# Kernel optimization log

Measured on AMD Instinct MI355X. Metric: run time of the kernel, lower is better.

## Reference

```python
import jax, jax.numpy as jnp
import numpy as np

N, IN, HID, OUT, HEADS = 50000, 128, 128, 16, 4
EL, EG = 800000, 200000
NEG_SLOPE = 0.2


def setup_inputs() -> dict:
    key = jax.random.key(0)
    ks = jax.random.split(key, 24)
    def gn(k, shape, fan_in):
        return (jax.random.normal(k, shape, jnp.float32) / np.sqrt(fan_in)).astype(jnp.float32)
    inp = {}
    inp['x'] = jax.random.normal(ks[0], (N, IN), jnp.float32)
    inp['local_edge_index'] = jax.random.randint(ks[1], (2, EL), 0, N, jnp.int64 if jax.config.jax_enable_x64 else jnp.int32)
    inp['global_edge_index'] = jax.random.randint(ks[2], (2, EG), 0, N, jnp.int64 if jax.config.jax_enable_x64 else jnp.int32)
    # local_processor: Linear(IN, HID)
    inp['W1'] = gn(ks[3], (IN, HID), IN); inp['b1'] = jnp.zeros((HID,), jnp.float32)
    # GCNConv(HID, HID): weight + bias
    inp['Wg'] = gn(ks[4], (HID, HID), HID); inp['bg'] = jnp.zeros((HID,), jnp.float32)
    # GATConv(HID, HID, heads=4, concat=False): lin to HEADS*HID, att vectors, bias of size HID
    inp['Wa'] = gn(ks[5], (HID, HEADS * HID), HID)
    inp['att_src'] = gn(ks[6], (HEADS, HID), HID)
    inp['att_dst'] = gn(ks[7], (HEADS, HID), HID)
    inp['ba'] = jnp.zeros((HID,), jnp.float32)
    # hierarchical_pool: Linear(2*HID, HID)
    inp['Wp'] = gn(ks[8], (2 * HID, HID), 2 * HID); inp['bp'] = jnp.zeros((HID,), jnp.float32)
    # classifier: Linear(HID, HID//2) -> ReLU -> Linear(HID//2, OUT)
    inp['Wc1'] = gn(ks[9], (HID, HID // 2), HID); inp['bc1'] = jnp.zeros((HID // 2,), jnp.float32)
    inp['Wc2'] = gn(ks[10], (HID // 2, OUT), HID // 2); inp['bc2'] = jnp.zeros((OUT,), jnp.float32)
    # uncertainty_head: Linear(HID, OUT)
    inp['Wu'] = gn(ks[11], (HID, OUT), HID); inp['bu'] = jnp.zeros((OUT,), jnp.float32)
    return inp


def _add_self_loops(ei, n):
    loop = jnp.arange(n, dtype=ei.dtype)
    return jnp.concatenate([ei[0], loop]), jnp.concatenate([ei[1], loop])


def gcn_conv(x, ei, W, b):
    n = x.shape[0]
    xw = x @ W                                        # [N, HID]
    src, dst = _add_self_loops(ei, n)
    deg = jax.ops.segment_sum(jnp.ones_like(dst, dtype=xw.dtype), dst, num_segments=n)
    dinv = jax.lax.rsqrt(jnp.maximum(deg, 1e-12))     # deg >= 1 thanks to self-loops
    norm = dinv[src] * dinv[dst]                      # [E+N]
    msg = xw[src] * norm[:, None]                     # gather + scale
    return jax.ops.segment_sum(msg, dst, num_segments=n) + b


def gat_conv(x, ei, W, att_src, att_dst, b):
    n = x.shape[0]
    h, c = att_src.shape
    xw = (x @ W).reshape(n, h, c)                     # [N, H, C]
    a_s = jnp.einsum('nhc,hc->nh', xw, att_src)       # [N, H]
    a_d = jnp.einsum('nhc,hc->nh', xw, att_dst)
    src, dst = _add_self_loops(ei, n)
    e = jax.nn.leaky_relu(a_s[src] + a_d[dst], NEG_SLOPE)   # [E+N, H]
    emax = jax.ops.segment_max(e, dst, num_segments=n)      # stable edge-softmax per dst
    ee = jnp.exp(e - emax[dst])
    denom = jax.ops.segment_sum(ee, dst, num_segments=n)
    alpha = ee / (denom[dst] + 1e-16)                        # [E+N, H]
    out = jax.ops.segment_sum(xw[src] * alpha[:, :, None], dst, num_segments=n)  # [N,H,C]
    return out.mean(axis=1) + b                              # concat=False -> head mean


def reference(x, local_edge_index, global_edge_index, W1, b1, Wg, bg, Wa, att_src, att_dst, ba, Wp, bp, Wc1, bc1, Wc2, bc2, Wu, bu):
    x_local = jax.nn.relu(x @ W1 + b1)                       # dropout is identity in eval
    x_lg = jax.nn.relu(gcn_conv(x_local, local_edge_index, Wg, bg))
    x_gg = jax.nn.relu(gat_conv(x_local, global_edge_index, Wa, att_src, att_dst, ba))
    x_comb = jnp.concatenate([x_lg, x_gg], axis=1)           # [N, 2*HID]
    x_pooled = jax.nn.relu(x_comb @ Wp + bp)
    x_final = x_pooled.mean(axis=0, keepdims=True)           # batch=None path
    prediction = jax.nn.relu(x_final @ Wc1 + bc1) @ Wc2 + bc2
    uncertainty = jax.nn.sigmoid(x_final @ Wu + bu)
    return prediction, uncertainty
```

## Files before the change

### kernel.cpp

```cpp
#include <hip/hip_runtime.h>
#include <hip/hip_bf16.h>

#define N_NODES 50000
#define F_IN 128
#define HID 128
#define N_OUT 16
#define HEADS 4
#define EL 800000
#define EG 200000
#define NEG_SLOPE 0.2f
#define NB 196
#define GB 391

typedef short bf16x8 __attribute__((ext_vector_type(8)));
typedef float f32x4 __attribute__((ext_vector_type(4)));
typedef float f32x2 __attribute__((ext_vector_type(2)));

static __device__ __forceinline__ float lrelu(float x) {
    return x > 0.f ? x : NEG_SLOPE * x;
}
static __device__ __forceinline__ unsigned short f2b(float f) {
    __hip_bfloat16 h = __float2bfloat16(f);
    return *reinterpret_cast<unsigned short*>(&h);
}
static __device__ __forceinline__ unsigned char f2fp8(float f) {
    unsigned pk = __builtin_amdgcn_cvt_pk_fp8_f32(f, f, 0, false);
    return (unsigned char)(pk & 0xFF);
}
static __device__ __forceinline__ f32x2 fp8x2_to_f32(unsigned u) {
    return __builtin_amdgcn_cvt_pk_f32_fp8((int)u, false);
}
static __device__ __forceinline__ float rdlane_f(float v, int l) {
    return __int_as_float(__builtin_amdgcn_readlane(__float_as_int(v), l));
}

__global__ __launch_bounds__(256) void conv_hist(
    const float* __restrict__ W1, unsigned short* __restrict__ W1t,
    const float* __restrict__ Wg, unsigned short* __restrict__ Wgt,
    const float* __restrict__ Wa, unsigned short* __restrict__ Wat,
    const float* __restrict__ Wp, unsigned short* __restrict__ Wpt,
    const int* __restrict__ ldst, const int* __restrict__ gdst, int* __restrict__ ghist)
{
    int b = blockIdx.x, t = threadIdx.x;
    if (b < 64) {
        int idx = b * 256 + t;
        int k = idx >> 7, n = idx & 127;
        W1t[n * 128 + k] = f2b(W1[idx]);
    } else if (b < 128) {
        int idx = (b - 64) * 256 + t;
        int k = idx >> 7, n = idx & 127;
        Wgt[n * 128 + k] = f2b(Wg[idx]);
    } else if (b < 384) {
        int idx = (b - 128) * 256 + t;
        int k = idx >> 9, n = idx & 511;
        Wat[(size_t)n * 128 + k] = f2b(Wa[idx]);
    } else if (b < 512) {
        int idx = (b - 384) * 256 + t;
        int k = idx >> 7, n = idx & 127;
        Wpt[(size_t)n * 256 + k] = f2b(Wp[idx]);
    } else {
        __shared__ int lh[NB];
        int blk = b - 512;
        bool loc = blk < 196;
        const int* dstp = loc ? ldst : gdst;
        int nE = loc ? EL : EG;
        int* gh = ghist + (loc ? 0 : NB);
        int start = (loc ? blk : blk - 196) * 4096;
        if (t < NB) lh[t] = 0;
        __syncthreads();
        #pragma unroll
        for (int i = 0; i < 16; i++) {
            int e = start + i * 256 + t;
            if (e < nE) atomicAdd(&lh[dstp[e] >> 8], 1);
        }
        __syncthreads();
        if (t < NB && lh[t]) atomicAdd(&gh[t], lh[t]);
    }
}

__global__ __launch_bounds__(256) void scan_gemmx(
    const int* __restrict__ ghist, int* __restrict__ bbase, int* __restrict__ gcur,
    const float* __restrict__ A, const unsigned short* __restrict__ Bt,
    const float* __restrict__ bias, unsigned short* __restrict__ out, int M)
{
    __shared__ unsigned short As[128 * 128];
    __shared__ unsigned short Bs[128 * 128];
    int tid = threadIdx.x;
    if (blockIdx.x < 2) {
        int* s = (int*)As;
        int g = blockIdx.x, t = tid;
        int v = (t < NB) ? ghist[g * NB + t] : 0;
        s[t] = v;
        __syncthreads();
        for (int off = 1; off < 256; off <<= 1) {
            int u = (t >= off) ? s[t - off] : 0;
            __syncthreads();
            s[t] += u;
            __syncthreads();
        }
        if (t < NB) {
            bbase[g * (NB + 1) + t] = s[t] - v;
            gcur[g * NB + t] = s[t] - v;
        }
        if (t == NB - 1) bbase[g * (NB + 1) + NB] = s[t];
        return;
    }
    int lane = tid & 63, w = tid >> 6;
    int wr = w >> 1, wc = w & 1;
    int l16 = lane & 15, lhi = lane >> 4;
    int m0 = (blockIdx.x - 2) * 128;
    f32x4 acc[4][4] = {};
    #pragma unroll
    for (int i = 0; i < 8; i++) {
        int u = tid + i * 256;
        int row = u >> 4, e0 = (u & 15) << 3;
        int sw = e0 ^ ((row & 7) << 3);
        int gr = m0 + row;
        unsigned short pb[8] = {};
        if (gr < M) {
            float4 a0 = *(const float4*)(A + (size_t)gr * 128 + e0);
            float4 a1 = *(const float4*)(A + (size_t)gr * 128 + e0 + 4);
            pb[0] = f2b(a0.x); pb[1] = f2b(a0.y); pb[2] = f2b(a0.z); pb[3] = f2b(a0.w);
            pb[4] = f2b(a1.x); pb[5] = f2b(a1.y); pb[6] = f2b(a1.z); pb[7] = f2b(a1.w);
        }
        *(bf16x8*)(As + row * 128 + sw) = *(bf16x8*)pb;
        bf16x8 vb = *(const bf16x8*)(Bt + (size_t)row * 128 + e0);
        *(bf16x8*)(Bs + row * 128 + sw) = vb;
    }
    __syncthreads();
    #pragma unroll
    for (int kk = 0; kk < 4; kk++) {
        int ke = kk * 32 + lhi * 8;
        bf16x8 af[4], bfr[4];
        #pragma unroll
        for (int m = 0; m < 4; m++) {
            int r = wr * 64 + m * 16 + l16;
            af[m] = *(const bf16x8*)(As + r * 128 + (ke ^ ((r & 7) << 3)));
        }
        #pragma unroll
        for (int n = 0; n < 4; n++) {
            int r = wc * 64 + n * 16 + l16;
            bfr[n] = *(const bf16x8*)(Bs + r * 128 + (ke ^ ((r & 7) << 3)));
        }
        #pragma unroll
        for (int m = 0; m < 4; m++)
            #pragma unroll
            for (int n = 0; n < 4; n++)
                acc[m][n] = __builtin_amdgcn_mfma_f32_16x16x32_bf16(af[m], bfr[n], acc[m][n], 0, 0, 0);
    }
    #pragma unroll
    for (int m = 0; m < 4; m++) {
        #pragma unroll
        for (int r = 0; r < 4; r++) {
            int row_g = m0 + wr * 64 + m * 16 + lhi * 4 + r;
            if (row_g >= M) continue;
            #pragma unroll
            for (int n = 0; n < 4; n++) {
                int col_g = wc * 64 + n * 16 + l16;
                float v = fmaxf(acc[m][n][r] + bias[col_g], 0.f);
                out[(size_t)row_g * 128 + col_g] = f2b(v);
            }
        }
    }
}

__global__ __launch_bounds__(256) void bucket_part(
    const int* __restrict__ lsrc, const int* __restrict__ ldst,
    const int* __restrict__ gsrc, const int* __restrict__ gdst,
    int* __restrict__ gcur, unsigned* __restrict__ ebuf_l, unsigned* __restrict__ ebuf_g)
{
    __shared__ int lhist[NB], lbase[NB];
    int blk = blockIdx.x, t = threadIdx.x;
    bool loc = blk < 196;
    const int* srcp = loc ? lsrc : gsrc;
    const int* dstp = loc ? ldst : gdst;
    int nE = loc ? EL : EG;
    unsigned* ebuf = loc ? ebuf_l : ebuf_g;
    int* cur = gcur + (loc ? 0 : NB);
    int start = (loc ? blk : blk - 196) * 4096;
    if (t < NB) lhist[t] = 0;
    __syncthreads();
    unsigned pk[16];
    #pragma unroll
    for (int i = 0; i < 16; i++) {
        int e = start + i * 256 + t;
        if (e < nE) {
            unsigned d = (unsigned)dstp[e];
            pk[i] = (d << 16) | (unsigned)srcp[e];
            atomicAdd(&lhist[d >> 8], 1);
        } else pk[i] = 0xFFFFFFFFu;
    }
    __syncthreads();
    if (t < NB) lbase[t] = atomicAdd(&cur[t], lhist[t]);
    __syncthreads();
    if (t < NB) lhist[t] = 0;
    __syncthreads();
    #pragma unroll
    for (int i = 0; i < 16; i++) {
        unsigned b = pk[i] >> 24;
        if (b < NB) {
            int r = atomicAdd(&lhist[b], 1);
            ebuf[lbase[b] + r] = pk[i];
        }
    }
}
__global__ __launch_bounds__(256) void bucket_csr(
    const unsigned* __restrict__ ebuf_l, const unsigned* __restrict__ ebuf_g,
    const int* __restrict__ bbase,
    int* __restrict__ offs_l, int* __restrict__ offs_g,
    unsigned short* __restrict__ csr_l, unsigned short* __restrict__ csr_g,
    float* __restrict__ dinv)
{
    __shared__ int cnt[256], s[256], cur[256];
    int blk = blockIdx.x, t = threadIdx.x;
    bool loc = blk < 196;
    int b = loc ? blk : blk - 196;
    const unsigned* ebuf = loc ? ebuf_l : ebuf_g;
    const int* bb = bbase + (loc ? 0 : NB + 1);
    int* offs = loc ? offs_l : offs_g;
    unsigned short* csr = loc ? csr_l : csr_g;
    int rs = bb[b], re = bb[b + 1];
    cnt[t] = 0;
    __syncthreads();
    for (int i = rs + t; i < re; i += 256) atomicAdd(&cnt[(ebuf[i] >> 16) & 255], 1);
    __syncthreads();
    int v = cnt[t];
    s[t] = v;
    __syncthreads();
    for (int off = 1; off < 256; off <<= 1) {
        int u = (t >= off) ? s[t - off] : 0;
        __syncthreads();
        s[t] += u;
        __syncthreads();
    }
    int excl = s[t] - v;
    int node = b * 256 + t;
    cur[t] = rs + excl;
    if (node < N_NODES) {
        offs[node] = rs + excl;
        if (loc) dinv[node] = rsqrtf((float)(v + 1));
    }
    if (blk == 0 && t == 0) offs_l[N_NODES] = EL;
    if (blk == 196 && t == 0) offs_g[N_NODES] = EG;
    __syncthreads();
    for (int i = rs + t; i < re; i += 256) {
        unsigned pk = ebuf[i];
        int r = atomicAdd(&cur[(pk >> 16) & 255], 1);
        csr[r] = (unsigned short)(pk & 0xFFFFu);
    }
}

__global__ __launch_bounds__(256) void gemm_gw5(
    const unsigned short* __restrict__ A, const unsigned short* __restrict__ Wgt,
    const unsigned short* __restrict__ Wat,
    unsigned char* __restrict__ xw_g8, unsigned char* __restrict__ xw_a8, int M,
    const float* __restrict__ atts, const float* __restrict__ attd,
    float* __restrict__ a_s, float* __restrict__ a_d,
    const float* __restrict__ dinv)
{
    __shared__ unsigned short As[128 * 128];
    __shared__ unsigned short Bs[128 * 128];
    __shared__ float sas[128], sad[128];
    int tid = threadIdx.x;
    int lane = tid & 63, w = tid >> 6;
    int wr = w >> 1, wc = w & 1;
    int l16 = lane & 15, lhi = lane >> 4;
    int m0 = blockIdx.x * 128;
    #pragma unroll
    for (int i = 0; i < 8; i++) {
        int u = tid + i * 256;
        int row = u >> 4, e0 = (u & 15) << 3;
        int sw = e0 ^ ((row & 7) << 3);
        bf16x8 va = {};
        int gr = m0 + row;
        if (gr < M) va = *(const bf16x8*)(A + (size_t)gr * 128 + e0);
        *(bf16x8*)(As + row * 128 + sw) = va;
    }
    for (int p = 0; p < 5; p++) {
        const unsigned short* Bt = (p == 0) ? Wgt : (Wat + (size_t)(p - 1) * 128 * 128);
        __syncthreads();
        #pragma unroll
        for (int i = 0; i < 8; i++) {
            int u = tid + i * 256;
            int row = u >> 4, e0 = (u & 15) << 3;
            int sw = e0 ^ ((row & 7) << 3);
            bf16x8 vb = *(const bf16x8*)(Bt + (size_t)row * 128 + e0);
            *(bf16x8*)(Bs + row * 128 + sw) = vb;
        }
        if (tid < 128) { sas[tid] = 0.f; sad[tid] = 0.f; }
        __syncthreads();
        f32x4 acc[4][4] = {};
        #pragma unroll
        for (int kk = 0; kk < 4; kk++) {
            int ke = kk * 32 + lhi * 8;
            bf16x8 af[4], bfr[4];
            #pragma unroll
            for (int m = 0; m < 4; m++) {
                int r = wr * 64 + m * 16 + l16;
                af[m] = *(const bf16x8*)(As + r * 128 + (ke ^ ((r & 7) << 3)));
            }
            #pragma unroll
            for (int n = 0; n < 4; n++) {
                int r = wc * 64 + n * 16 + l16;
                bfr[n] = *(const bf16x8*)(Bs + r * 128 + (ke ^ ((r & 7) << 3)));
            }
            #pragma unroll
            for (int m = 0; m < 4; m++)
                #pragma unroll
                for (int n = 0; n < 4; n++)
                    acc[m][n] = __builtin_amdgcn_mfma_f32_16x16x32_bf16(af[m], bfr[n], acc[m][n], 0, 0, 0);
        }
        if (p == 0) {
            #pragma unroll
            for (int m = 0; m < 4; m++)
                #pragma unroll
                for (int r = 0; r < 4; r++) {
                    int row_g = m0 + wr * 64 + m * 16 + lhi * 4 + r;
                    if (row_g >= M) continue;
                    float dv = dinv[row_g];
                    #pragma unroll
                    for (int n = 0; n < 4; n++) {
                        int col_g = wc * 64 + n * 16 + l16;
                        xw_g8[(size_t)row_g * 128 + col_g] = f2fp8(acc[m][n][r] * dv);
                    }
                }
        } else {
            int head = p - 1;
            float ats[4], atd[4];
            #pragma unroll
            for (int n = 0; n < 4; n++) {
                int cl = wc * 64 + n * 16 + l16;
                ats[n] = atts[head * 128 + cl];
                atd[n] = attd[head * 128 + cl];
            }
            #pragma unroll
            for (int m = 0; m < 4; m++) {
                #pragma unroll
                for (int r = 0; r < 4; r++) {
                    int row_l = wr * 64 + m * 16 + lhi * 4 + r;
                    int row_g = m0 + row_l;
                    float ps = 0.f, pd = 0.f;
                    #pragma unroll
                    for (int n = 0; n < 4; n++) {
                        float v = acc[m][n][r];
                        ps = fmaf(v, ats[n], ps);
                        pd = fmaf(v, atd[n], pd);
                        if (row_g < M) {
                            int col_g = head * 128 + wc * 64 + n * 16 + l16;
                            xw_a8[(size_t)row_g * 512 + col_g] = f2fp8(v);
                        }
                    }
                    #pragma unroll
                    for (int off = 1; off < 16; off <<= 1) {
                        ps += __shfl_xor(ps, off);
                        pd += __shfl_xor(pd, off);
                    }
                    if (l16 == 0) {
                        atomicAdd(&sas[row_l], ps);
                        atomicAdd(&sad[row_l], pd);
                    }
                }
            }
            __syncthreads();
            if (tid < 128) {
                int row_g = m0 + tid;
                if (row_g < M) {
                    a_s[(size_t)row_g * 4 + head] = sas[tid];
                    a_d[(size_t)row_g * 4 + head] = sad[tid];
                }
            }
        }
    }
}

__global__ __launch_bounds__(256) void fused_gather(
    const int* __restrict__ offs_l, const unsigned short* __restrict__ csr_l,
    const unsigned char* __restrict__ xw_g8, const float* __restrict__ dinv,
    const float* __restrict__ bg,
    const int* __restrict__ offs_g, const unsigned short* __restrict__ csr_g,
    const float* __restrict__ a_s, const float* __restrict__ a_d,
    const unsigned char* __restrict__ xw_a8, const float* __restrict__ ba,
    unsigned short* __restrict__ xcomb)
{
    int blk = blockIdx.x;
    int tid = threadIdx.x;
    int lane = tid & 63;
    int g = lane >> 4, q = lane & 15;
    if (blk < 12500) {
        int d = (blk * 256 + tid) >> 6;
        if (d >= N_NODES) return;
        int base = offs_l[d], end = offs_l[d + 1];
        unsigned goff = (unsigned)q * 8u;
        f32x2 a0 = {0.f, 0.f}, a1 = {0.f, 0.f}, a2 = {0.f, 0.f}, a3 = {0.f, 0.f};
        for (int i = base; i < end; ) {
            int chunk = min(64, end - i);
            int sv = (lane < chunk) ? (int)csr_l[i + lane] : 0;
            int nst = (chunk + 3) >> 2;
            int j = 0;
            for (; j + 2 <= nst; j += 2) {
                int eA = j * 4 + g, eB = eA + 4;
                int sA = __shfl(sv, eA);
                int sB = __shfl(sv, eB);
                float mkA = (eA < chunk) ? 1.f : 0.f;
                float mkB = (eB < chunk) ? 1.f : 0.f;
                uint2 vA = *(const uint2*)(xw_g8 + (((unsigned)sA) << 7) + goff);
                uint2 vB = *(const uint2*)(xw_g8 + (((unsigned)sB) << 7) + goff);
                f32x2 mA = {mkA, mkA}, mB = {mkB, mkB};
                a0 += __builtin_amdgcn_cvt_pk_f32_fp8((int)vA.x, false) * mA;
                a1 += __builtin_amdgcn_cvt_pk_f32_fp8((int)vA.x, true) * mA;
                a2 += __builtin_amdgcn_cvt_pk_f32_fp8((int)vA.y, false) * mA;
                a3 += __builtin_amdgcn_cvt_pk_f32_fp8((int)vA.y, true) * mA;
                a0 += __builtin_amdgcn_cvt_pk_f32_fp8((int)vB.x, false) * mB;
                a1 += __builtin_amdgcn_cvt_pk_f32_fp8((int)vB.x, true) * mB;
                a2 += __builtin_amdgcn_cvt_pk_f32_fp8((int)vB.y, false) * mB;
                a3 += __builtin_amdgcn_cvt_pk_f32_fp8((int)vB.y, true) * mB;
            }
            for (; j < nst; j++) {
                int e = j * 4 + g;
                int s = __shfl(sv, e);
                float mk = (e < chunk) ? 1.f : 0.f;
                f32x2 m2 = {mk, mk};
                uint2 v = *(const uint2*)(xw_g8 + (((unsigned)s) << 7) + goff);
                a0 += __builtin_amdgcn_cvt_pk_f32_fp8((int)v.x, false) * m2;
                a1 += __builtin_amdgcn_cvt_pk_f32_fp8((int)v.x, true) * m2;
                a2 += __builtin_amdgcn_cvt_pk_f32_fp8((int)v.y, false) * m2;
                a3 += __builtin_amdgcn_cvt_pk_f32_fp8((int)v.y, true) * m2;
            }
            i += chunk;
        }
        float av[8] = {a0[0], a0[1], a1[0], a1[1], a2[0], a2[1], a3[0], a3[1]};
        #pragma unroll
        for (int k = 0; k < 8; k++) {
            av[k] += __shfl_xor(av[k], 16);
            av[k] += __shfl_xor(av[k], 32);
        }
        if (g == 0) {
            float dd = dinv[d];
            uint2 sv2 = *(const uint2*)(xw_g8 + (((unsigned)d) << 7) + goff);
            f32x2 s0 = fp8x2_to_f32(sv2.x & 0xFFFFu);
            f32x2 s1 = __builtin_amdgcn_cvt_pk_f32_fp8((int)sv2.x, true);
            f32x2 s2 = fp8x2_to_f32(sv2.y & 0xFFFFu);
            f32x2 s3 = __builtin_amdgcn_cvt_pk_f32_fp8((int)sv2.y, true);
            float sf[8] = {s0[0], s0[1], s1[0], s1[1], s2[0], s2[1], s3[0], s3[1]};
            float4 b0 = *(const float4*)(bg + q * 8);
            float4 b1 = *(const float4*)(bg + q * 8 + 4);
            float bb[8] = {b0.x, b0.y, b0.z, b0.w, b1.x, b1.y, b1.z, b1.w};
            unsigned o[4];
            #pragma unroll
            for (int k = 0; k < 4; k++) {
                float v0 = fmaxf(dd * (av[2 * k] + sf[2 * k]) + bb[2 * k], 0.f);
                float v1 = fmaxf(dd * (av[2 * k + 1] + sf[2 * k + 1]) + bb[2 * k + 1], 0.f);
                o[k] = (unsigned)f2b(v0) | ((unsigned)f2b(v1) << 16);
            }
            *(uint4*)(xcomb + (size_t)d * 256 + q * 8) = make_uint4(o[0], o[1], o[2], o[3]);
        }
    } else {
        int d = ((blk - 12500) * 256 + tid) >> 6;
        if (d >= N_NODES) return;
        int base = offs_g[d], end = offs_g[d + 1];
        int deg = end - base;
        if (deg <= 16) {
            float ad_g = a_d[(size_t)d * 4 + g];
            float es = lrelu(a_s[(size_t)d * 4 + g] + ad_g);
            int sv = (q < deg) ? (int)csr_g[base + q] : 0;
            float asg = a_s[(size_t)sv * 4 + g];
            float e = (q < deg) ? lrelu(asg + ad_g) : -1e30f;
            float m = e;
            m = fmaxf(m, __shfl_xor(m, 1));
            m = fmaxf(m, __shfl_xor(m, 2));
            m = fmaxf(m, __shfl_xor(m, 4));
            m = fmaxf(m, __shfl_xor(m, 8));
            m = fmaxf(m, es);
            float wgt = (q < deg) ? __expf(e - m) : 0.f;
            float den = wgt;
            den += __shfl_xor(den, 1);
            den += __shfl_xor(den, 2);
            den += __shfl_xor(den, 4);
            den += __shfl_xor(den, 8);
            float se = __expf(es - m);
            den += se;
            float rinv = 0.25f / (den + 1e-16f);
            float wf = wgt * rinv;
            float selfw = se * rinv;
            unsigned goff = (unsigned)(g * 128 + q * 8);
            int b48 = lane & 48;
            f32x2 a0 = {0.f, 0.f}, a1 = {0.f, 0.f}, a2 = {0.f, 0.f}, a3 = {0.f, 0.f};
            int j = 0;
            for (; j + 2 <= deg; j += 2) {
                int sA = __builtin_amdgcn_readlane(sv, j);
                int sB = __builtin_amdgcn_readlane(sv, j + 1);
                float alA = __shfl(wf, b48 + j);
                float alB = __shfl(wf, b48 + j + 1);
                uint2 vA = *(const uint2*)(xw_a8 + (((unsigned)sA) << 9) + goff);
                uint2 vB = *(const uint2*)(xw_a8 + (((unsigned)sB) << 9) + goff);
                f32x2 mA = {alA, alA}, mB = {alB, alB};
                a0 += __builtin_amdgcn_cvt_pk_f32_fp8((int)vA.x, false) * mA;
                a1 += __builtin_amdgcn_cvt_pk_f32_fp8((int)vA.x, true) * mA;
                a2 += __builtin_amdgcn_cvt_pk_f32_fp8((int)vA.y, false) * mA;
                a3 += __builtin_amdgcn_cvt_pk_f32_fp8((int)vA.y, true) * mA;
                a0 += __builtin_amdgcn_cvt_pk_f32_fp8((int)vB.x, false) * mB;
                a1 += __builtin_amdgcn_cvt_pk_f32_fp8((int)vB.x, true) * mB;
                a2 += __builtin_amdgcn_cvt_pk_f32_fp8((int)vB.y, false) * mB;
                a3 += __builtin_amdgcn_cvt_pk_f32_fp8((int)vB.y, true) * mB;
            }
            if (j < deg) {
                int sA = __builtin_amdgcn_readlane(sv, j);
                float alA = __shfl(wf, b48 + j);
                uint2 vA = *(const uint2*)(xw_a8 + (((unsigned)sA) << 9) + goff);
                f32x2 mA = {alA, alA};
                a0 += __builtin_amdgcn_cvt_pk_f32_fp8((int)vA.x, false) * mA;
                a1 += __builtin_amdgcn_cvt_pk_f32_fp8((int)vA.x, true) * mA;
                a2 += __builtin_amdgcn_cvt_pk_f32_fp8((int)vA.y, false) * mA;
                a3 += __builtin_amdgcn_cvt_pk_f32_fp8((int)vA.y, true) * mA;
            }
            {
                uint2 v = *(const uint2*)(xw_a8 + (((unsigned)d) << 9) + goff);
                f32x2 ms = {selfw, selfw};
                a0 += __builtin_amdgcn_cvt_pk_f32_fp8((int)v.x, false) * ms;
                a1 += __builtin_amdgcn_cvt_pk_f32_fp8((int)v.x, true) * ms;
                a2 += __builtin_amdgcn_cvt_pk_f32_fp8((int)v.y, false) * ms;
                a3 += __builtin_amdgcn_cvt_pk_f32_fp8((int)v.y, true) * ms;
            }
            float av[8] = {a0[0], a0[1], a1[0], a1[1], a2[0], a2[1], a3[0], a3[1]};
            #pragma unroll
            for (int k = 0; k < 8; k++) {
                av[k] += __shfl_xor(av[k], 16);
                av[k] += __shfl_xor(av[k], 32);
            }
            if (g == 0) {
                float4 b0 = *(const float4*)(ba + q * 8);
                float4 b1 = *(const float4*)(ba + q * 8 + 4);
                float bb[8] = {b0.x, b0.y, b0.z, b0.w, b1.x, b1.y, b1.z, b1.w};
                unsigned o[4];
                #pragma unroll
                for (int k = 0; k < 4; k++) {
                    float v0 = fmaxf(av[2 * k] + bb[2 * k], 0.f);
                    float v1 = fmaxf(av[2 * k + 1] + bb[2 * k + 1], 0.f);
                    o[k] = (unsigned)f2b(v0) | ((unsigned)f2b(v1) << 16);
                }
                *(uint4*)(xcomb + (size_t)d * 256 + 128 + q * 8) = make_uint4(o[0], o[1], o[2], o[3]);
            }
            return;
        }
        float4 ad4 = *(const float4*)(a_d + (size_t)d * 4);
        float4 asd = *(const float4*)(a_s + (size_t)d * 4);
        float es0 = lrelu(asd.x + ad4.x), es1 = lrelu(asd.y + ad4.y);
        float es2 = lrelu(asd.z + ad4.z), es3 = lrelu(asd.w + ad4.w);
        if (deg <= 64) {
            int sv = 0;
            float e0 = -1e30f, e1 = -1e30f, e2 = -1e30f, e3 = -1e30f;
            if (lane < deg) {
                sv = csr_g[base + lane];
                float4 s4 = *(const float4*)(a_s + (size_t)sv * 4);
                e0 = lrelu(s4.x + ad4.x); e1 = lrelu(s4.y + ad4.y);
                e2 = lrelu(s4.z + ad4.z); e3 = lrelu(s4.w + ad4.w);
            }
            float m0 = e0, m1 = e1, m2 = e2, m3 = e3;
            #pragma unroll
            for (int off = 1; off < 64; off <<= 1) {
                m0 = fmaxf(m0, __shfl_xor(m0, off));
                m1 = fmaxf(m1, __shfl_xor(m1, off));
                m2 = fmaxf(m2, __shfl_xor(m2, off));
                m3 = fmaxf(m3, __shfl_xor(m3, off));
            }
            m0 = fmaxf(m0, es0); m1 = fmaxf(m1, es1);
            m2 = fmaxf(m2, es2); m3 = fmaxf(m3, es3);
            float w0 = (lane < deg) ? __expf(e0 - m0) : 0.f;
            float w1 = (lane < deg) ? __expf(e1 - m1) : 0.f;
            float w2 = (lane < deg) ? __expf(e2 - m2) : 0.f;
            float w3 = (lane < deg) ? __expf(e3 - m3) : 0.f;
            float d0 = w0, d1 = w1, d2 = w2, d3 = w3;
            #pragma unroll
            for (int off = 1; off < 64; off <<= 1) {
                d0 += __shfl_xor(d0, off); d1 += __shfl_xor(d1, off);
                d2 += __shfl_xor(d2, off); d3 += __shfl_xor(d3, off);
            }
            d0 += __expf(es0 - m0); d1 += __expf(es1 - m1);
            d2 += __expf(es2 - m2); d3 += __expf(es3 - m3);
            float r0 = 0.25f / (d0 + 1e-16f), r1 = 0.25f / (d1 + 1e-16f);
            float r2 = 0.25f / (d2 + 1e-16f), r3 = 0.25f / (d3 + 1e-16f);
            w0 *= r0; w1 *= r1; w2 *= r2; w3 *= r3;
            float wsel = (g == 0) ? w0 : (g == 1) ? w1 : (g == 2) ? w2 : w3;
            float selfw = (g == 0) ? __expf(es0 - m0) * r0 : (g == 1) ? __expf(es1 - m1) * r1
                        : (g == 2) ? __expf(es2 - m2) * r2 : __expf(es3 - m3) * r3;
            unsigned goff = (unsigned)(g * 128 + q * 8);
            f32x2 a0 = {0.f, 0.f}, a1 = {0.f, 0.f}, a2 = {0.f, 0.f}, a3 = {0.f, 0.f};
            for (int j = 0; j < deg; j++) {
                int s = __builtin_amdgcn_readlane(sv, j);
                float al = rdlane_f(wsel, j);
                uint2 v = *(const uint2*)(xw_a8 + (((unsigned)s) << 9) + goff);
                f32x2 mA = {al, al};
                a0 += __builtin_amdgcn_cvt_pk_f32_fp8((int)v.x, false) * mA;
                a1 += __builtin_amdgcn_cvt_pk_f32_fp8((int)v.x, true) * mA;
                a2 += __builtin_amdgcn_cvt_pk_f32_fp8((int)v.y, false) * mA;
                a3 += __builtin_amdgcn_cvt_pk_f32_fp8((int)v.y, true) * mA;
            }
            {
                uint2 v = *(const uint2*)(xw_a8 + (((unsigned)d) << 9) + goff);
                f32x2 ms = {selfw, selfw};
                a0 += __builtin_amdgcn_cvt_pk_f32_fp8((int)v.x, false) * ms;
                a1 += __builtin_amdgcn_cvt_pk_f32_fp8((int)v.x, true) * ms;
                a2 += __builtin_amdgcn_cvt_pk_f32_fp8((int)v.y, false) * ms;
                a3 += __builtin_amdgcn_cvt_pk_f32_fp8((int)v.y, true) * ms;
            }
            float av[8] = {a0[0], a0[1], a1[0], a1[1], a2[0], a2[1], a3[0], a3[1]};
            #pragma unroll
            for (int k = 0; k < 8; k++) {
                av[k] += __shfl_xor(av[k], 16);
                av[k] += __shfl_xor(av[k], 32);
            }
            if (g == 0) {
                float4 b0 = *(const float4*)(ba + q * 8);
                float4 b1 = *(const float4*)(ba + q * 8 + 4);
                float bb[8] = {b0.x, b0.y, b0.z, b0.w, b1.x, b1.y, b1.z, b1.w};
                unsigned o[4];
                #pragma unroll
                for (int k = 0; k < 4; k++) {
                    float v0 = fmaxf(av[2 * k] + bb[2 * k], 0.f);
                    float v1 = fmaxf(av[2 * k + 1] + bb[2 * k + 1], 0.f);
                    o[k] = (unsigned)f2b(v0) | ((unsigned)f2b(v1) << 16);
                }
                *(uint4*)(xcomb + (size_t)d * 256 + 128 + q * 8) = make_uint4(o[0], o[1], o[2], o[3]);
            }
        } else {
            int c2 = lane * 2;
            const unsigned short* xa = (const unsigned short*)xw_a8;
            float m0 = es0, m1 = es1, m2 = es2, m3 = es3;
            for (int i = base; i < end; i += 64) {
                int c = min(64, end - i);
                float t0 = -1e30f, t1 = -1e30f, t2 = -1e30f, t3 = -1e30f;
                if (lane < c) {
                    int s = csr_g[i + lane];
                    float4 s4 = *(const float4*)(a_s + (size_t)s * 4);
                    t0 = lrelu(s4.x + ad4.x); t1 = lrelu(s4.y + ad4.y);
                    t2 = lrelu(s4.z + ad4.z); t3 = lrelu(s4.w + ad4.w);
                }
                m0 = fmaxf(m0, t0); m1 = fmaxf(m1, t1);
                m2 = fmaxf(m2, t2); m3 = fmaxf(m3, t3);
            }
            #pragma unroll
            for (int off = 1; off < 64; off <<= 1) {
                m0 = fmaxf(m0, __shfl_xor(m0, off));
                m1 = fmaxf(m1, __shfl_xor(m1, off));
                m2 = fmaxf(m2, __shfl_xor(m2, off));
                m3 = fmaxf(m3, __shfl_xor(m3, off));
            }
            float d0 = 0.f, d1 = 0.f, d2 = 0.f, d3 = 0.f;
            for (int i = base; i < end; i += 64) {
                int c = min(64, end - i);
                if (lane < c) {
                    int s = csr_g[i + lane];
                    float4 s4 = *(const float4*)(a_s + (size_t)s * 4);
                    d0 += __expf(lrelu(s4.x + ad4.x) - m0);
                    d1 += __expf(lrelu(s4.y + ad4.y) - m1);
                    d2 += __expf(lrelu(s4.z + ad4.z) - m2);
                    d3 += __expf(lrelu(s4.w + ad4.w) - m3);
                }
            }
            #pragma unroll
            for (int off = 1; off < 64; off <<= 1) {
                d0 += __shfl_xor(d0, off); d1 += __shfl_xor(d1, off);
                d2 += __shfl_xor(d2, off); d3 += __shfl_xor(d3, off);
            }
            d0 += __expf(es0 - m0); d1 += __expf(es1 - m1);
            d2 += __expf(es2 - m2); d3 += __expf(es3 - m3);
            float r0 = 1.f / (d0 + 1e-16f), r1 = 1.f / (d1 + 1e-16f);
            float r2 = 1.f / (d2 + 1e-16f), r3 = 1.f / (d3 + 1e-16f);
            float ax = 0.f, ay = 0.f;
            for (int i = base; i < end; i += 64) {
                int c = min(64, end - i);
                int sv = 0;
                float w0 = 0.f, w1 = 0.f, w2 = 0.f, w3 = 0.f;
                if (lane < c) {
                    sv = csr_g[i + lane];
                    float4 s4 = *(const float4*)(a_s + (size_t)sv * 4);
                    w0 = __expf(lrelu(s4.x + ad4.x) - m0) * r0;
                    w1 = __expf(lrelu(s4.y + ad4.y) - m1) * r1;
                    w2 = __expf(lrelu(s4.z + ad4.z) - m2) * r2;
                    w3 = __expf(lrelu(s4.w + ad4.w) - m3) * r3;
                }
                for (int j = 0; j < c; j++) {
                    int s = __shfl(sv, j);
                    float a0 = __shfl(w0, j), a1 = __shfl(w1, j);
                    float a2 = __shfl(w2, j), a3 = __shfl(w3, j);
                    const unsigned short* row = xa + (size_t)s * 256 + lane;
                    f32x2 v0 = fp8x2_to_f32(row[0]);
                    f32x2 v1 = fp8x2_to_f32(row[64]);
                    f32x2 v2 = fp8x2_to_f32(row[128]);
                    f32x2 v3 = fp8x2_to_f32(row[192]);
                    ax = fmaf(v0[0], a0, ax); ay = fmaf(v0[1], a0, ay);
                    ax = fmaf(v1[0], a1, ax); ay = fmaf(v1[1], a1, ay);
                    ax = fmaf(v2[0], a2, ax); ay = fmaf(v2[1], a2, ay);
                    ax = fmaf(v3[0], a3, ax); ay = fmaf(v3[1], a3, ay);
                }
            }
            float s0 = __expf(es0 - m0) * r0, s1 = __expf(es1 - m1) * r1;
            float s2 = __expf(es2 - m2) * r2, s3 = __expf(es3 - m3) * r3;
            const unsigned short* row = xa + (size_t)d * 256 + lane;
            f32x2 v0 = fp8x2_to_f32(row[0]);
            f32x2 v1 = fp8x2_to_f32(row[64]);
            f32x2 v2 = fp8x2_to_f32(row[128]);
            f32x2 v3 = fp8x2_to_f32(row[192]);
            ax = fmaf(v0[0], s0, ax); ay = fmaf(v0[1], s0, ay);
            ax = fmaf(v1[0], s1, ax); ay = fmaf(v1[1], s1, ay);
            ax = fmaf(v2[0], s2, ax); ay = fmaf(v2[1], s2, ay);
            ax = fmaf(v3[0], s3, ax); ay = fmaf(v3[1], s3, ay);
            float ox = fmaxf(0.25f * ax + ba[c2], 0.f);
            float oy = fmaxf(0.25f * ay + ba[c2 + 1], 0.f);
            unsigned uo = (unsigned)f2b(ox) | ((unsigned)f2b(oy) << 16);
            *(unsigned*)(xcomb + (size_t)d * 256 + 128 + c2) = uo;
        }
    }
}

__global__ __launch_bounds__(256) void mfma_pool(
    const unsigned short* __restrict__ A, const unsigned short* __restrict__ Bt,
    const float* __restrict__ bp, float* __restrict__ sumvec, int M)
{
    __shared__ unsigned short As[128 * 128];
    __shared__ unsigned short Bs[128 * 128];
    __shared__ float red[128];
    int tid = threadIdx.x;
    int lane = tid & 63, w = tid >> 6;
    int wr = w >> 1, wc = w & 1;
    int l16 = lane & 15, lhi = lane >> 4;
    int m0 = blockIdx.x * 128;
    f32x4 acc[4][4] = {};
    for (int kb = 0; kb < 256; kb += 128) {
        if (kb) __syncthreads();
        #pragma unroll
        for (int i = 0; i < 8; i++) {
            int u = tid + i * 256;
            int row = u >> 4, e0 = (u & 15) << 3;
            int sw = e0 ^ ((row & 7) << 3);
            bf16x8 va = {};
            int gr = m0 + row;
            if (gr < M) va = *(const bf16x8*)(A + (size_t)gr * 256 + kb + e0);
            *(bf16x8*)(As + row * 128 + sw) = va;
            bf16x8 vb = *(const bf16x8*)(Bt + (size_t)row * 256 + kb + e0);
            *(bf16x8*)(Bs + row * 128 + sw) = vb;
        }
        __syncthreads();
        #pragma unroll
        for (int kk = 0; kk < 4; kk++) {
            int ke = kk * 32 + lhi * 8;
            bf16x8 af[4], bfr[4];
            #pragma unroll
            for (int m = 0; m < 4; m++) {
                int r = wr * 64 + m * 16 + l16;
                af[m] = *(const bf16x8*)(As + r * 128 + (ke ^ ((r & 7) << 3)));
            }
            #pragma unroll
            for (int n = 0; n < 4; n++) {
                int r = wc * 64 + n * 16 + l16;
                bfr[n] = *(const bf16x8*)(Bs + r * 128 + (ke ^ ((r & 7) << 3)));
            }
            #pragma unroll
            for (int m = 0; m < 4; m++)
                #pragma unroll
                for (int n = 0; n < 4; n++)
                    acc[m][n] = __builtin_amdgcn_mfma_f32_16x16x32_bf16(af[m], bfr[n], acc[m][n], 0, 0, 0);
        }
    }
    float bcol[4];
    #pragma unroll
    for (int n = 0; n < 4; n++) bcol[n] = bp[wc * 64 + n * 16 + l16];
    float colsum[4] = {0.f, 0.f, 0.f, 0.f};
    #pragma unroll
    for (int m = 0; m < 4; m++) {
        #pragma unroll
        for (int r = 0; r < 4; r++) {
            int row_g = m0 + wr * 64 + m * 16 + lhi * 4 + r;
            if (row_g < M) {
                #pragma unroll
                for (int n = 0; n < 4; n++)
                    colsum[n] += fmaxf(acc[m][n][r] + bcol[n], 0.f);
            }
        }
    }
    #pragma unroll
    for (int n = 0; n < 4; n++) {
        colsum[n] += __shfl_xor(colsum[n], 16);
        colsum[n] += __shfl_xor(colsum[n], 32);
    }
    if (tid < 128) red[tid] = 0.f;
    __syncthreads();
    if (lhi == 0) {
        #pragma unroll
        for (int n = 0; n < 4; n++)
            atomicAdd(&red[wc * 64 + n * 16 + l16], colsum[n]);
    }
    __syncthreads();
    if (tid < 128) atomicAdd(&sumvec[tid], red[tid]);
}

__global__ void final_head(const float* __restrict__ sumvec,
                           const float* __restrict__ Wc1, const float* __restrict__ bc1,
                           const float* __restrict__ Wc2, const float* __restrict__ bc2,
                           const float* __restrict__ Wu, const float* __restrict__ bu,
                           float* __restrict__ out)
{
    __shared__ float xf[128];
    __shared__ float h1[64];
    int t = threadIdx.x;
    xf[t] = sumvec[t] * (1.0f / N_NODES);
    __syncthreads();
    if (t < 64) {
        float s = bc1[t];
        for (int c = 0; c < 128; c++) s = fmaf(xf[c], Wc1[c * 64 + t], s);
        h1[t] = fmaxf(s, 0.f);
    }
    __syncthreads();
    if (t < 16) {
        float s = bc2[t];
        for (int j = 0; j < 64; j++) s = fmaf(h1[j], Wc2[j * 16 + t], s);
        out[t] = s;
        float u = bu[t];
        for (int c = 0; c < 128; c++) u = fmaf(xf[c], Wu[c * 16 + t], u);
        out[16 + t] = 1.0f / (1.0f + expf(-u));
    }
}

extern "C" void kernel_launch(void* const* d_in, const int* in_sizes, int n_in,
                              void* d_out, int out_size, void* d_ws, size_t ws_size,
                              hipStream_t stream) {
    const float* x    = (const float*)d_in[0];
    const int*   lei  = (const int*)d_in[1];
    const int*   gei  = (const int*)d_in[2];
    const float* W1   = (const float*)d_in[3];
    const float* b1   = (const float*)d_in[4];
    const float* Wg   = (const float*)d_in[5];
    const float* bg   = (const float*)d_in[6];
    const float* Wa   = (const float*)d_in[7];
    const float* atts = (const float*)d_in[8];
    const float* attd = (const float*)d_in[9];
    const float* ba   = (const float*)d_in[10];
    const float* Wp   = (const float*)d_in[11];
    const float* bp   = (const float*)d_in[12];
    const float* Wc1  = (const float*)d_in[13];
    const float* bc1  = (const float*)d_in[14];
    const float* Wc2  = (const float*)d_in[15];
    const float* bc2  = (const float*)d_in[16];
    const float* Wu   = (const float*)d_in[17];
    const float* bu   = (const float*)d_in[18];

    const int* lsrc = lei;
    const int* ldst = lei + EL;
    const int* gsrc = gei;
    const int* gdst = gei + EG;

    uintptr_t base = (uintptr_t)d_ws;
    auto alloc = [&](size_t bytes) { void* p = (void*)base; base += (bytes + 255) & ~(size_t)255; return p; };
    unsigned short* x_loc  = (unsigned short*)alloc((size_t)N_NODES * 128 * 2);
    unsigned char*  xw_g8  = (unsigned char*)alloc((size_t)N_NODES * 128);
    unsigned char*  xw_a8  = (unsigned char*)alloc((size_t)N_NODES * 512);
    unsigned short* xcomb  = (unsigned short*)alloc((size_t)N_NODES * 256 * 2);
    unsigned short* W1t    = (unsigned short*)alloc((size_t)128 * 128 * 2);
    unsigned short* Wgt    = (unsigned short*)alloc((size_t)128 * 128 * 2);
    unsigned short* Wat    = (unsigned short*)alloc((size_t)512 * 128 * 2);
    unsigned short* Wpt    = (unsigned short*)alloc((size_t)128 * 256 * 2);
    float* dinv       = (float*)alloc((size_t)N_NODES * 4);
    float* a_s        = (float*)alloc((size_t)N_NODES * 4 * 4);
    float* a_d        = (float*)alloc((size_t)N_NODES * 4 * 4);
    int*   ghist      = (int*)alloc((size_t)2 * NB * 4);
    int*   bbase      = (int*)alloc((size_t)2 * (NB + 1) * 4);
    int*   gcur       = (int*)alloc((size_t)2 * NB * 4);
    unsigned* ebuf_l  = (unsigned*)alloc((size_t)EL * 4);
    unsigned* ebuf_g  = (unsigned*)alloc((size_t)EG * 4);
    int*   offs_l     = (int*)alloc(((size_t)N_NODES + 1) * 4);
    int*   offs_g     = (int*)alloc(((size_t)N_NODES + 1) * 4);
    unsigned short* csr_l = (unsigned short*)alloc((size_t)EL * 2);
    unsigned short* csr_g = (unsigned short*)alloc((size_t)EG * 2);
    float* sumvec     = (float*)alloc(128 * 4);

    hipMemsetAsync(ghist, 0, (size_t)2 * NB * 4, stream);
    hipMemsetAsync(sumvec, 0, 128 * 4, stream);

    conv_hist<<<757, 256, 0, stream>>>(W1, W1t, Wg, Wgt, Wa, Wat, Wp, Wpt,
                                       ldst, gdst, ghist);
    scan_gemmx<<<393, 256, 0, stream>>>(ghist, bbase, gcur, x, W1t, b1, x_loc, N_NODES);
    bucket_part<<<245, 256, 0, stream>>>(lsrc, ldst, gsrc, gdst, gcur, ebuf_l, ebuf_g);
    bucket_csr<<<392, 256, 0, stream>>>(ebuf_l, ebuf_g, bbase, offs_l, offs_g,
                                        csr_l, csr_g, dinv);
    gemm_gw5<<<GB, 256, 0, stream>>>(x_loc, Wgt, Wat, xw_g8, xw_a8, N_NODES,
                                     atts, attd, a_s, a_d, dinv);
    fused_gather<<<25000, 256, 0, stream>>>(offs_l, csr_l, xw_g8, dinv, bg,
                                            offs_g, csr_g, a_s, a_d, xw_a8, ba, xcomb);
    mfma_pool<<<GB, 256, 0, stream>>>(xcomb, Wpt, bp, sumvec, N_NODES);
    final_head<<<1, 128, 0, stream>>>(sumvec, Wc1, bc1, Wc2, bc2, Wu, bu,
                                      (float*)d_out);
}
```

Before: 172.3 us.

## Merge edge bucketing with GEMM launch, defer dinv scaling, fuse final head

The edge-partition kernel now runs as extra blocks inside the GEMM launch, so bucketing and the GCN/GAT projection execute concurrently instead of back to back. To remove the GEMM's dependence on dinv, the GEMM writes unscaled fp8 xw_g, and bucket_csr rescales it in place per node after computing the degree. This adds an extra fp8 read-modify-write pass over xw_g with a second quantization step. The final classifier head is folded into the pool kernel through a last-block counter, which removes one launch.

```diff
diff --git a/kernel.cpp b/kernel.cpp
--- a/kernel.cpp
+++ b/kernel.cpp
@@ -164,104 +164,58 @@
     }
 }
 
-__global__ __launch_bounds__(256) void bucket_part(
-    const int* __restrict__ lsrc, const int* __restrict__ ldst,
-    const int* __restrict__ gsrc, const int* __restrict__ gdst,
-    int* __restrict__ gcur, unsigned* __restrict__ ebuf_l, unsigned* __restrict__ ebuf_g)
-{
-    __shared__ int lhist[NB], lbase[NB];
-    int blk = blockIdx.x, t = threadIdx.x;
-    bool loc = blk < 196;
-    const int* srcp = loc ? lsrc : gsrc;
-    const int* dstp = loc ? ldst : gdst;
-    int nE = loc ? EL : EG;
-    unsigned* ebuf = loc ? ebuf_l : ebuf_g;
-    int* cur = gcur + (loc ? 0 : NB);
-    int start = (loc ? blk : blk - 196) * 4096;
-    if (t < NB) lhist[t] = 0;
-    __syncthreads();
-    unsigned pk[16];
-    #pragma unroll
-    for (int i = 0; i < 16; i++) {
-        int e = start + i * 256 + t;
-        if (e < nE) {
-            unsigned d = (unsigned)dstp[e];
-            pk[i] = (d << 16) | (unsigned)srcp[e];
-            atomicAdd(&lhist[d >> 8], 1);
-        } else pk[i] = 0xFFFFFFFFu;
-    }
-    __syncthreads();
-    if (t < NB) lbase[t] = atomicAdd(&cur[t], lhist[t]);
-    __syncthreads();
-    if (t < NB) lhist[t] = 0;
-    __syncthreads();
-    #pragma unroll
-    for (int i = 0; i < 16; i++) {
-        unsigned b = pk[i] >> 24;
-        if (b < NB) {
-            int r = atomicAdd(&lhist[b], 1);
-            ebuf[lbase[b] + r] = pk[i];
-        }
-    }
-}
-__global__ __launch_bounds__(256) void bucket_csr(
-    const unsigned* __restrict__ ebuf_l, const unsigned* __restrict__ ebuf_g,
-    const int* __restrict__ bbase,
-    int* __restrict__ offs_l, int* __restrict__ offs_g,
-    unsigned short* __restrict__ csr_l, unsigned short* __restrict__ csr_g,
-    float* __restrict__ dinv)
-{
-    __shared__ int cnt[256], s[256], cur[256];
-    int blk = blockIdx.x, t = threadIdx.x;
-    bool loc = blk < 196;
-    int b = loc ? blk : blk - 196;
-    const unsigned* ebuf = loc ? ebuf_l : ebuf_g;
-    const int* bb = bbase + (loc ? 0 : NB + 1);
-    int* offs = loc ? offs_l : offs_g;
-    unsigned short* csr = loc ? csr_l : csr_g;
-    int rs = bb[b], re = bb[b + 1];
-    cnt[t] = 0;
-    __syncthreads();
-    for (int i = rs + t; i < re; i += 256) atomicAdd(&cnt[(ebuf[i] >> 16) & 255], 1);
-    __syncthreads();
-    int v = cnt[t];
-    s[t] = v;
-    __syncthreads();
-    for (int off = 1; off < 256; off <<= 1) {
-        int u = (t >= off) ? s[t - off] : 0;
-        __syncthreads();
-        s[t] += u;
-        __syncthreads();
-    }
-    int excl = s[t] - v;
-    int node = b * 256 + t;
-    cur[t] = rs + excl;
-    if (node < N_NODES) {
-        offs[node] = rs + excl;
-        if (loc) dinv[node] = rsqrtf((float)(v + 1));
-    }
-    if (blk == 0 && t == 0) offs_l[N_NODES] = EL;
-    if (blk == 196 && t == 0) offs_g[N_NODES] = EG;
-    __syncthreads();
-    for (int i = rs + t; i < re; i += 256) {
-        unsigned pk = ebuf[i];
-        int r = atomicAdd(&cur[(pk >> 16) & 255], 1);
-        csr[r] = (unsigned short)(pk & 0xFFFFu);
-    }
-}
-
-__global__ __launch_bounds__(256) void gemm_gw5(
+__global__ __launch_bounds__(256) void part_gw5(
     const unsigned short* __restrict__ A, const unsigned short* __restrict__ Wgt,
     const unsigned short* __restrict__ Wat,
     unsigned char* __restrict__ xw_g8, unsigned char* __restrict__ xw_a8, int M,
     const float* __restrict__ atts, const float* __restrict__ attd,
     float* __restrict__ a_s, float* __restrict__ a_d,
-    const float* __restrict__ dinv)
+    const int* __restrict__ lsrc, const int* __restrict__ ldst,
+    const int* __restrict__ gsrc, const int* __restrict__ gdst,
+    int* __restrict__ gcur, unsigned* __restrict__ ebuf_l, unsigned* __restrict__ ebuf_g)
 {
     __shared__ unsigned short As[128 * 128];
     __shared__ unsigned short Bs[128 * 128];
     __shared__ float sas[128], sad[128];
     int tid = threadIdx.x;
+    if (blockIdx.x >= GB) {
+        int* lhist = (int*)As;
+        int* lbase = ((int*)As) + 256;
+        int blk = blockIdx.x - GB, t = tid;
+        bool loc = blk < 196;
+        const int* srcp = loc ? lsrc : gsrc;
+        const int* dstp = loc ? ldst : gdst;
+        int nE = loc ? EL : EG;
+        unsigned* ebuf = loc ? ebuf_l : ebuf_g;
+        int* cur = gcur + (loc ? 0 : NB);
+        int start = (loc ? blk : blk - 196) * 4096;
+        if (t < NB) lhist[t] = 0;
+        __syncthreads();
+        unsigned pk[16];
+        #pragma unroll
+        for (int i = 0; i < 16; i++) {
+            int e = start + i * 256 + t;
+            if (e < nE) {
+                unsigned d = (unsigned)dstp[e];
+                pk[i] = (d << 16) | (unsigned)srcp[e];
+                atomicAdd(&lhist[d >> 8], 1);
+            } else pk[i] = 0xFFFFFFFFu;
+        }
+        __syncthreads();
+        if (t < NB) lbase[t] = atomicAdd(&cur[t], lhist[t]);
+        __syncthreads();
+        if (t < NB) lhist[t] = 0;
+        __syncthreads();
+        #pragma unroll
+        for (int i = 0; i < 16; i++) {
+            unsigned b = pk[i] >> 24;
+            if (b < NB) {
+                int r = atomicAdd(&lhist[b], 1);
+                ebuf[lbase[b] + r] = pk[i];
+            }
+        }
+        return;
+    }
     int lane = tid & 63, w = tid >> 6;
     int wr = w >> 1, wc = w & 1;
     int l16 = lane & 15, lhi = lane >> 4;
@@ -317,11 +271,10 @@
                 for (int r = 0; r < 4; r++) {
                     int row_g = m0 + wr * 64 + m * 16 + lhi * 4 + r;
                     if (row_g >= M) continue;
-                    float dv = dinv[row_g];
                     #pragma unroll
                     for (int n = 0; n < 4; n++) {
                         int col_g = wc * 64 + n * 16 + l16;
-                        xw_g8[(size_t)row_g * 128 + col_g] = f2fp8(acc[m][n][r] * dv);
+                        xw_g8[(size_t)row_g * 128 + col_g] = f2fp8(acc[m][n][r]);
                     }
                 }
         } else {
@@ -369,6 +322,71 @@
                     a_d[(size_t)row_g * 4 + head] = sad[tid];
                 }
             }
+        }
+    }
+}
+
+__global__ __launch_bounds__(256) void bucket_csr(
+    const unsigned* __restrict__ ebuf_l, const unsigned* __restrict__ ebuf_g,
+    const int* __restrict__ bbase,
+    int* __restrict__ offs_l, int* __restrict__ offs_g,
+    unsigned short* __restrict__ csr_l, unsigned short* __restrict__ csr_g,
+    float* __restrict__ dinv, unsigned* __restrict__ xwg32)
+{
+    __shared__ int cnt[256], s[256], cur[256];
+    __shared__ float sdinv[256];
+    int blk = blockIdx.x, t = threadIdx.x;
+    bool loc = blk < 196;
+    int b = loc ? blk : blk - 196;
+    const unsigned* ebuf = loc ? ebuf_l : ebuf_g;
+    const int* bb = bbase + (loc ? 0 : NB + 1);
+    int* offs = loc ? offs_l : offs_g;
+    unsigned short* csr = loc ? csr_l : csr_g;
+    int rs = bb[b], re = bb[b + 1];
+    cnt[t] = 0;
+    __syncthreads();
+    for (int i = rs + t; i < re; i += 256) atomicAdd(&cnt[(ebuf[i] >> 16) & 255], 1);
+    __syncthreads();
+    int v = cnt[t];
+    s[t] = v;
+    __syncthreads();
+    for (int off = 1; off < 256; off <<= 1) {
+        int u = (t >= off) ? s[t - off] : 0;
+        __syncthreads();
+        s[t] += u;
+        __syncthreads();
+    }
+    int excl = s[t] - v;
+    int node = b * 256 + t;
+    cur[t] = rs + excl;
+    float dv = rsqrtf((float)(v + 1));
+    if (node < N_NODES) {
+        offs[node] = rs + excl;
+        if (loc) dinv[node] = dv;
+    }
+    sdinv[t] = dv;
+    if (blk == 0 && t == 0) offs_l[N_NODES] = EL;
+    if (blk == 196 && t == 0) offs_g[N_NODES] = EG;
+    __syncthreads();
+    for (int i = rs + t; i < re; i += 256) {
+        unsigned pk = ebuf[i];
+        int r = atomicAdd(&cur[(pk >> 16) & 255], 1);
+        csr[r] = (unsigned short)(pk & 0xFFFFu);
+    }
+    if (loc) {
+        size_t base_u = (size_t)b * 256 * 32;
+        for (int u = t; u < 256 * 32; u += 256) {
+            int nl = u >> 5;
+            int nodeg = b * 256 + nl;
+            if (nodeg >= N_NODES) break;
+            unsigned wv = xwg32[base_u + u];
+            f32x2 lo = __builtin_amdgcn_cvt_pk_f32_fp8((int)wv, false);
+            f32x2 hi = __builtin_amdgcn_cvt_pk_f32_fp8((int)wv, true);
+            float dvn = sdinv[nl];
+            lo *= dvn; hi *= dvn;
+            unsigned pk2 = __builtin_amdgcn_cvt_pk_fp8_f32(lo[0], lo[1], 0, false);
+            pk2 = __builtin_amdgcn_cvt_pk_fp8_f32(hi[0], hi[1], pk2, true);
+            xwg32[base_u + u] = pk2;
         }
     }
 }
@@ -713,13 +731,19 @@
     }
 }
 
-__global__ __launch_bounds__(256) void mfma_pool(
+__global__ __launch_bounds__(256) void mfma_pool_head(
     const unsigned short* __restrict__ A, const unsigned short* __restrict__ Bt,
-    const float* __restrict__ bp, float* __restrict__ sumvec, int M)
+    const float* __restrict__ bp, float* __restrict__ sumvec, int* __restrict__ counter,
+    int M,
+    const float* __restrict__ Wc1, const float* __restrict__ bc1,
+    const float* __restrict__ Wc2, const float* __restrict__ bc2,
+    const float* __restrict__ Wu, const float* __restrict__ bu,
+    float* __restrict__ out)
 {
     __shared__ unsigned short As[128 * 128];
     __shared__ unsigned short Bs[128 * 128];
     __shared__ float red[128];
+    __shared__ int lastflag;
     int tid = threadIdx.x;
     int lane = tid & 63, w = tid >> 6;
     int wr = w >> 1, wc = w & 1;
@@ -792,32 +816,28 @@
     }
     __syncthreads();
     if (tid < 128) atomicAdd(&sumvec[tid], red[tid]);
-}
-
-__global__ void final_head(const float* __restrict__ sumvec,
-                           const float* __restrict__ Wc1, const float* __restrict__ bc1,
-                           const float* __restrict__ Wc2, const float* __restrict__ bc2,
-                           const float* __restrict__ Wu, const float* __restrict__ bu,
-                           float* __restrict__ out)
-{
+    __threadfence();
+    __syncthreads();
+    if (tid == 0) lastflag = (atomicAdd(counter, 1) == (int)gridDim.x - 1);
+    __syncthreads();
+    if (!lastflag) return;
     __shared__ float xf[128];
     __shared__ float h1[64];
-    int t = threadIdx.x;
-    xf[t] = sumvec[t] * (1.0f / N_NODES);
-    __syncthreads();
-    if (t < 64) {
-        float s = bc1[t];
-        for (int c = 0; c < 128; c++) s = fmaf(xf[c], Wc1[c * 64 + t], s);
-        h1[t] = fmaxf(s, 0.f);
-    }
-    __syncthreads();
-    if (t < 16) {
-        float s = bc2[t];
-        for (int j = 0; j < 64; j++) s = fmaf(h1[j], Wc2[j * 16 + t], s);
-        out[t] = s;
-        float u = bu[t];
-        for (int c = 0; c < 128; c++) u = fmaf(xf[c], Wu[c * 16 + t], u);
-        out[16 + t] = 1.0f / (1.0f + expf(-u));
+    if (tid < 128) xf[tid] = atomicAdd(&sumvec[tid], 0.f) * (1.0f / N_NODES);
+    __syncthreads();
+    if (tid < 64) {
+        float s = bc1[tid];
+        for (int c = 0; c < 128; c++) s = fmaf(xf[c], Wc1[c * 64 + tid], s);
+        h1[tid] = fmaxf(s, 0.f);
+    }
+    __syncthreads();
+    if (tid < 16) {
+        float s = bc2[tid];
+        for (int j = 0; j < 64; j++) s = fmaf(h1[j], Wc2[j * 16 + tid], s);
+        out[tid] = s;
+        float u = bu[tid];
+        for (int c = 0; c < 128; c++) u = fmaf(xf[c], Wu[c * 16 + tid], u);
+        out[16 + tid] = 1.0f / (1.0f + expf(-u));
     }
 }
 
@@ -871,22 +891,22 @@
     int*   offs_g     = (int*)alloc(((size_t)N_NODES + 1) * 4);
     unsigned short* csr_l = (unsigned short*)alloc((size_t)EL * 2);
     unsigned short* csr_g = (unsigned short*)alloc((size_t)EG * 2);
-    float* sumvec     = (float*)alloc(128 * 4);
+    float* sumvec     = (float*)alloc(128 * 4 + 256);
+    int*   counter    = (int*)(sumvec + 128);
 
     hipMemsetAsync(ghist, 0, (size_t)2 * NB * 4, stream);
-    hipMemsetAsync(sumvec, 0, 128 * 4, stream);
+    hipMemsetAsync(sumvec, 0, 128 * 4 + 4, stream);
 
     conv_hist<<<757, 256, 0, stream>>>(W1, W1t, Wg, Wgt, Wa, Wat, Wp, Wpt,
                                        ldst, gdst, ghist);
     scan_gemmx<<<393, 256, 0, stream>>>(ghist, bbase, gcur, x, W1t, b1, x_loc, N_NODES);
-    bucket_part<<<245, 256, 0, stream>>>(lsrc, ldst, gsrc, gdst, gcur, ebuf_l, ebuf_g);
+    part_gw5<<<GB + 245, 256, 0, stream>>>(x_loc, Wgt, Wat, xw_g8, xw_a8, N_NODES,
+                                           atts, attd, a_s, a_d,
+                                           lsrc, ldst, gsrc, gdst, gcur, ebuf_l, ebuf_g);
     bucket_csr<<<392, 256, 0, stream>>>(ebuf_l, ebuf_g, bbase, offs_l, offs_g,
-                                        csr_l, csr_g, dinv);
-    gemm_gw5<<<GB, 256, 0, stream>>>(x_loc, Wgt, Wat, xw_g8, xw_a8, N_NODES,
-                                     atts, attd, a_s, a_d, dinv);
+                                        csr_l, csr_g, dinv, (unsigned*)xw_g8);
     fused_gather<<<25000, 256, 0, stream>>>(offs_l, csr_l, xw_g8, dinv, bg,
                                             offs_g, csr_g, a_s, a_d, xw_a8, ba, xcomb);
-    mfma_pool<<<GB, 256, 0, stream>>>(xcomb, Wpt, bp, sumvec, N_NODES);
-    final_head<<<1, 128, 0, stream>>>(sumvec, Wc1, bc1, Wc2, bc2, Wu, bu,
-                                      (float*)d_out);
-}
+    mfma_pool_head<<<GB, 256, 0, stream>>>(xcomb, Wpt, bp, sumvec, counter, N_NODES,
+                                           Wc1, bc1, Wc2, bc2, Wu, bu, (float*)d_out);
+}
```

Result: slower. 206.7 us (+19.9%).
